# Performance work log

Measured on AMD Instinct MI355X. Metric: run time of the kernel, lower is better.

Reference implementation:

```python
import jax, jax.numpy as jnp
import numpy as np

N_NODES = 150000
N_EDGES = 2400000


def gcn_conv(x, W, b, src, dst, n):
    """PyG GCNConv: add self-loops, symmetric D^-1/2 A_hat D^-1/2 norm, x@W then scatter-sum, + bias."""
    h = x @ W  # [N, out]
    loop = jnp.arange(n)
    s = jnp.concatenate([src, loop])
    d = jnp.concatenate([dst, loop])
    deg = jax.ops.segment_sum(jnp.ones(s.shape, dtype=h.dtype), d, num_segments=n)
    dis = jnp.where(deg > 0, jax.lax.rsqrt(jnp.maximum(deg, 1e-12)), 0.0)
    norm = dis[s] * dis[d]  # [E+N]
    out = jax.ops.segment_sum(h[s] * norm[:, None], d, num_segments=n)
    return out + b


def setup_inputs() -> dict:
    key = jax.random.key(0)
    ks = jax.random.split(key, 16)
    d = 32
    inp = {
        "x": jax.random.normal(ks[0], (N_NODES, 2), dtype=jnp.float32),
        "edge_index": jax.random.randint(ks[1], (2, N_EDGES), 0, N_NODES, dtype=jnp.int64),
        "fc1_w": jax.random.normal(ks[2], (2, d), dtype=jnp.float32) * 0.5,
        "fc1_b": jax.random.normal(ks[3], (d,), dtype=jnp.float32) * 0.1,
        "conv1_w": jax.random.normal(ks[4], (d, d), dtype=jnp.float32) * (1.0 / np.sqrt(d)),
        "conv1_b": jax.random.normal(ks[5], (d,), dtype=jnp.float32) * 0.1,
        "conv2_w": jax.random.normal(ks[6], (d, d), dtype=jnp.float32) * (1.0 / np.sqrt(d)),
        "conv2_b": jax.random.normal(ks[7], (d,), dtype=jnp.float32) * 0.1,
        "conv31_w": jax.random.normal(ks[8], (d, d), dtype=jnp.float32) * (1.0 / np.sqrt(d)),
        "conv31_b": jax.random.normal(ks[9], (d,), dtype=jnp.float32) * 0.1,
        "conv32_w": jax.random.normal(ks[10], (d, d), dtype=jnp.float32) * (1.0 / np.sqrt(d)),
        "conv32_b": jax.random.normal(ks[11], (d,), dtype=jnp.float32) * 0.1,
        "fc21_w": jax.random.normal(ks[12], (d, 1), dtype=jnp.float32) * (1.0 / np.sqrt(d)),
        "fc21_b": jax.random.normal(ks[13], (1,), dtype=jnp.float32) * 0.1,
        "fc22_w": jax.random.normal(ks[14], (d, 1), dtype=jnp.float32) * (1.0 / np.sqrt(d)),
        "fc22_b": jax.random.normal(ks[15], (1,), dtype=jnp.float32) * 0.1,
    }
    return inp


def reference(x, edge_index, fc1_w, fc1_b, conv1_w, conv1_b, conv2_w, conv2_b,
              conv31_w, conv31_b, conv32_w, conv32_b, fc21_w, fc21_b, fc22_w, fc22_b):
    n = x.shape[0]
    src, dst = edge_index[0], edge_index[1]
    h = jax.nn.relu(x @ fc1_w + fc1_b)
    h = jax.nn.relu(gcn_conv(h, conv1_w, conv1_b, src, dst, n))
    h = jax.nn.relu(gcn_conv(h, conv2_w, conv2_b, src, dst, n))
    x1 = jax.nn.relu(gcn_conv(h, conv31_w, conv31_b, src, dst, n)) @ fc21_w + fc21_b
    x2 = jax.nn.relu(gcn_conv(h, conv32_w, conv32_b, src, dst, n)) @ fc22_w + fc22_b
    return jnp.concatenate([x1, x2], axis=1)  # [N, 2]
```

## Files before the change

### kernel.cpp

```cpp
#include <hip/hip_runtime.h>

#define N_NODES 150000
#define N_EDGES 2400000
#define D 32
#define NBUCK 1172
#define CHUNK 4096
#define NCHK 586
#define CSR_CAP (N_EDGES + 3 * N_NODES + 64)

__global__ __launch_bounds__(256) void kA_hist(const int* __restrict__ dst,
                                               int* __restrict__ cnt) {
    __shared__ int bins[NBUCK];
    int t = threadIdx.x;
    for (int k = t; k < NBUCK; k += 256) bins[k] = 0;
    __syncthreads();
    int e0 = blockIdx.x * CHUNK;
#pragma unroll
    for (int r = 0; r < CHUNK / 256; ++r) {
        int e = e0 + r * 256 + t;
        if (e < N_EDGES) atomicAdd(&bins[dst[e] >> 7], 1);
    }
    __syncthreads();
    for (int k = t; k < NBUCK; k += 256) cnt[blockIdx.x * NBUCK + k] = bins[k];
}

__global__ __launch_bounds__(256) void kS1(int* __restrict__ cnt, int* __restrict__ bstart) {
    __shared__ int tile[8][33];
    __shared__ int carry[32];
    int t = threadIdx.x;
    int tl = t & 31, tr = t >> 5;
    int b = blockIdx.x * 32 + tl;
    if (t < 32) carry[t] = 0;
    __syncthreads();
    for (int c0 = 0; c0 < NCHK; c0 += 8) {
        int c = c0 + tr;
        int v = (c < NCHK && b < NBUCK) ? cnt[c * NBUCK + b] : 0;
        tile[tr][tl] = v;
        __syncthreads();
        if (t < 32) {
            int s = carry[t];
#pragma unroll
            for (int r = 0; r < 8; ++r) { int x = tile[r][t]; tile[r][t] = s; s += x; }
            carry[t] = s;
        }
        __syncthreads();
        if (c < NCHK && b < NBUCK) cnt[c * NBUCK + b] = tile[tr][tl];
        __syncthreads();
    }
    if (t < 32 && b < NBUCK) bstart[b] = carry[t];
}

__global__ void k_scan_small(int* __restrict__ a, int m) {
    __shared__ int s[256];
    __shared__ int carry;
    int t = threadIdx.x;
    if (t == 0) carry = 0;
    __syncthreads();
    for (int base = 0; base < m; base += 256) {
        int v = (base + t < m) ? a[base + t] : 0;
        s[t] = v;
        __syncthreads();
        for (int off = 1; off < 256; off <<= 1) {
            int add = (t >= off) ? s[t - off] : 0;
            __syncthreads();
            s[t] += add;
            __syncthreads();
        }
        int c0 = carry;
        if (base + t < m) a[base + t] = c0 + s[t] - v;
        int bsum = s[255];
        __syncthreads();
        if (t == 0) carry = c0 + bsum;
        __syncthreads();
    }
    if (t == 0) a[m] = carry;
}

__global__ __launch_bounds__(256) void kB_scatter(const int* __restrict__ src,
                                                  const int* __restrict__ dst,
                                                  const int* __restrict__ cnt,
                                                  const int* __restrict__ bstart,
                                                  int* __restrict__ ebuf) {
    __shared__ int lofs[NBUCK];
    int t = threadIdx.x;
    for (int k = t; k < NBUCK; k += 256)
        lofs[k] = bstart[k] + cnt[blockIdx.x * NBUCK + k];
    __syncthreads();
    int e0 = blockIdx.x * CHUNK;
#pragma unroll
    for (int r = 0; r < CHUNK / 256; ++r) {
        int e = e0 + r * 256 + t;
        if (e < N_EDGES) {
            int d = dst[e];
            int p = atomicAdd(&lofs[d >> 7], 1);
            ebuf[p] = src[e] | ((d & 127) << 18);
        }
    }
}

__global__ __launch_bounds__(256) void kC1(const int* __restrict__ ebuf,
                                           const int* __restrict__ bstart,
                                           const float2* __restrict__ x,
                                           int* __restrict__ deg,
                                           float* __restrict__ dis,
                                           float4* __restrict__ xd,
                                           int* __restrict__ pbase) {
    __shared__ int hist[128];
    __shared__ int sc[128];
    int b = blockIdx.x, t = threadIdx.x;
    if (t < 128) hist[t] = 0;
    __syncthreads();
    int s0 = bstart[b], s1 = bstart[b + 1];
    for (int e = s0 + t; e < s1; e += 256) atomicAdd(&hist[ebuf[e] >> 18], 1);
    __syncthreads();
    int i = b * 128 + t;
    if (t < 128) {
        int dv = hist[t];
        if (i < N_NODES) {
            deg[i] = dv;
            float dz = rsqrtf((float)dv + 1.0f);
            dis[i] = dz;
            float2 xv = x[i];
            xd[i] = make_float4(xv.x, xv.y, dz, 0.f);
        } else if (i == N_NODES) {
            xd[i] = make_float4(0.f, 0.f, 0.f, 0.f);
        }
        sc[t] = (i < N_NODES) ? ((dv + 3) & ~3) : 0;
    }
    __syncthreads();
    for (int s = 64; s > 0; s >>= 1) {
        if (t < s) sc[t] += sc[t + s];
        __syncthreads();
    }
    if (t == 0) pbase[b] = sc[0];
}

__global__ __launch_bounds__(256) void kC3(const int* __restrict__ ebuf,
                                           const int* __restrict__ bstart,
                                           const int* __restrict__ deg,
                                           const int* __restrict__ pbase,
                                           int* __restrict__ csr,
                                           int* __restrict__ irow,
                                           float* __restrict__ HA,
                                           float* __restrict__ HB) {
    __shared__ int sc[128];
    __shared__ int loff[128];
    __shared__ int pos[128];
    int b = blockIdx.x, t = threadIdx.x;
    if (b == 0) {
        if (t == 0) irow[N_NODES] = pbase[NBUCK];
        if (t < 64) csr[pbase[NBUCK] + t] = N_NODES;
        if (t >= 64 && t < 96) HA[(size_t)N_NODES * D + (t - 64)] = 0.f;
        if (t >= 96 && t < 128) HB[(size_t)N_NODES * D + (t - 96)] = 0.f;
    }
    int i = b * 128 + t;
    int dv = 0, pad = 0;
    if (t < 128) {
        dv = (i < N_NODES) ? deg[i] : 0;
        pad = (dv + 3) & ~3;
        sc[t] = pad;
        pos[t] = 0;
    }
    __syncthreads();
    for (int off = 1; off < 128; off <<= 1) {
        int add = 0;
        if (t < 128 && t >= off) add = sc[t - off];
        __syncthreads();
        if (t < 128) sc[t] += add;
        __syncthreads();
    }
    int base = pbase[b];
    if (t < 128) {
        loff[t] = sc[t] - pad;
        if (i < N_NODES) irow[i] = base + loff[t];
    }
    __syncthreads();
    int s0 = bstart[b], s1 = bstart[b + 1];
    for (int e = s0 + t; e < s1; e += 256) {
        int v = ebuf[e];
        int dl = v >> 18;
        int p = atomicAdd(&pos[dl], 1);
        csr[base + loff[dl] + p] = v & 0x3FFFF;
    }
    __syncthreads();
    if (t < 128 && i < N_NODES) {
        int st = base + loff[t] + dv, en = base + loff[t] + pad;
        for (int q = st; q < en; ++q) csr[q] = N_NODES;
    }
}

__global__ __launch_bounds__(256) void k_layer1f(const float4* __restrict__ xd,
                                                 const int* __restrict__ row,
                                                 const int* __restrict__ csr,
                                                 const float* __restrict__ W,
                                                 const float* __restrict__ bf,
                                                 const float* __restrict__ Wc,
                                                 const float* __restrict__ bc,
                                                 float* __restrict__ hout) {
    __shared__ float4 stage[8][16];
    __shared__ float arow[8][32];
    int g = threadIdx.x >> 5, l = threadIdx.x & 31, f = l;
    int t = blockIdx.x * 256 + threadIdx.x;
    int i = t >> 5;
    if (i >= N_NODES) return;
    float w0 = W[f], w1 = W[D + f], bb = bf[f];
    float wcol[D];
#pragma unroll
    for (int k = 0; k < D; ++k) wcol[k] = Wc[k * D + f];
    float4 sv = xd[i];
    float hs = fmaf(sv.x, w0, fmaf(sv.y, w1, bb));
    hs = hs > 0.f ? hs : 0.f;
    float a = hs * sv.z;
    int rs = row[i], re = row[i + 1];
    int j0 = rs;
    int cs = csr[j0 + (l & 15)];
    while (j0 < re) {
        int nxt = csr[j0 + 16 + (l & 15)];
        if (l < 16) {
            int s2 = (j0 + l < re) ? cs : N_NODES;
            stage[g][l] = xd[s2];
        }
#pragma unroll
        for (int it = 0; it < 4; ++it) {
            if (j0 + it * 4 >= re) break;
            float4 v0 = stage[g][it * 4 + 0];
            float4 v1 = stage[g][it * 4 + 1];
            float4 v2 = stage[g][it * 4 + 2];
            float4 v3 = stage[g][it * 4 + 3];
            float h0 = fmaf(v0.x, w0, fmaf(v0.y, w1, bb)); h0 = h0 > 0.f ? h0 : 0.f;
            float h1 = fmaf(v1.x, w0, fmaf(v1.y, w1, bb)); h1 = h1 > 0.f ? h1 : 0.f;
            float h2 = fmaf(v2.x, w0, fmaf(v2.y, w1, bb)); h2 = h2 > 0.f ? h2 : 0.f;
            float h3 = fmaf(v3.x, w0, fmaf(v3.y, w1, bb)); h3 = h3 > 0.f ? h3 : 0.f;
            a = fmaf(h0, v0.z, a);
            a = fmaf(h1, v1.z, a);
            a = fmaf(h2, v2.z, a);
            a = fmaf(h3, v3.z, a);
        }
        cs = nxt;
        j0 += 16;
    }
    float di = sv.z;
    a *= di;
    arow[g][f] = a;
    float acc = 0.f;
#pragma unroll
    for (int q = 0; q < 8; ++q) {
        float4 aq = ((const float4*)arow[g])[q];
        acc = fmaf(aq.x, wcol[4 * q + 0],
              fmaf(aq.y, wcol[4 * q + 1],
              fmaf(aq.z, wcol[4 * q + 2],
              fmaf(aq.w, wcol[4 * q + 3], acc))));
    }
    float v = acc + bc[f];
    v = v > 0.f ? v : 0.f;
    hout[t] = v * di;
}

__global__ __launch_bounds__(256) void k_layer(const float* __restrict__ hsc,
                                               const int* __restrict__ row,
                                               const int* __restrict__ csr,
                                               const float* __restrict__ dis,
                                               const float* __restrict__ W,
                                               const float* __restrict__ b,
                                               float* __restrict__ hout) {
    __shared__ float arow[16][32];
    int g = threadIdx.x >> 5, l = threadIdx.x & 31, f = l;
    int gg = blockIdx.x * 8 + g;
    int iA = gg * 2, iB = iA + 1;
    float wcol[D];
#pragma unroll
    for (int k = 0; k < D; ++k) wcol[k] = W[k * D + f];
    int c = l & 7, l16 = l & 15, sub = l >> 3;
    const float4* rowf4 = (const float4*)hsc;
    int rsA = row[iA], mid = row[iB], reB = row[iB + 1];
    float4 aA = make_float4(0.f, 0.f, 0.f, 0.f);
    float4 aB = make_float4(0.f, 0.f, 0.f, 0.f);
    int jA = rsA, jB = mid;
    int csA = csr[jA + l16], csB = csr[jB + l16];
    while (jA < mid && jB < reB) {
        int nA = csr[jA + 16 + l16], nB = csr[jB + 16 + l16];
        float4 vA[4], vB[4];
#pragma unroll
        for (int it = 0; it < 4; ++it)
            if (jA + it * 4 < mid) { int s = __shfl(csA, it * 4 + sub, 32); vA[it] = rowf4[s * 8 + c]; }
#pragma unroll
        for (int it = 0; it < 4; ++it)
            if (jB + it * 4 < reB) { int s = __shfl(csB, it * 4 + sub, 32); vB[it] = rowf4[s * 8 + c]; }
#pragma unroll
        for (int it = 0; it < 4; ++it) {
            if (jA + it * 4 < mid) { aA.x += vA[it].x; aA.y += vA[it].y; aA.z += vA[it].z; aA.w += vA[it].w; }
            if (jB + it * 4 < reB) { aB.x += vB[it].x; aB.y += vB[it].y; aB.z += vB[it].z; aB.w += vB[it].w; }
        }
        csA = nA; csB = nB; jA += 16; jB += 16;
    }
    while (jA < mid) {
        int nA = csr[jA + 16 + l16];
        float4 vA[4];
#pragma unroll
        for (int it = 0; it < 4; ++it)
            if (jA + it * 4 < mid) { int s = __shfl(csA, it * 4 + sub, 32); vA[it] = rowf4[s * 8 + c]; }
#pragma unroll
        for (int it = 0; it < 4; ++it)
            if (jA + it * 4 < mid) { aA.x += vA[it].x; aA.y += vA[it].y; aA.z += vA[it].z; aA.w += vA[it].w; }
        csA = nA; jA += 16;
    }
    while (jB < reB) {
        int nB = csr[jB + 16 + l16];
        float4 vB[4];
#pragma unroll
        for (int it = 0; it < 4; ++it)
            if (jB + it * 4 < reB) { int s = __shfl(csB, it * 4 + sub, 32); vB[it] = rowf4[s * 8 + c]; }
#pragma unroll
        for (int it = 0; it < 4; ++it)
            if (jB + it * 4 < reB) { aB.x += vB[it].x; aB.y += vB[it].y; aB.z += vB[it].z; aB.w += vB[it].w; }
        csB = nB; jB += 16;
    }
    aA.x += __shfl_xor(aA.x, 8, 32);  aA.y += __shfl_xor(aA.y, 8, 32);
    aA.z += __shfl_xor(aA.z, 8, 32);  aA.w += __shfl_xor(aA.w, 8, 32);
    aA.x += __shfl_xor(aA.x, 16, 32); aA.y += __shfl_xor(aA.y, 16, 32);
    aA.z += __shfl_xor(aA.z, 16, 32); aA.w += __shfl_xor(aA.w, 16, 32);
    aB.x += __shfl_xor(aB.x, 8, 32);  aB.y += __shfl_xor(aB.y, 8, 32);
    aB.z += __shfl_xor(aB.z, 8, 32);  aB.w += __shfl_xor(aB.w, 8, 32);
    aB.x += __shfl_xor(aB.x, 16, 32); aB.y += __shfl_xor(aB.y, 16, 32);
    aB.z += __shfl_xor(aB.z, 16, 32); aB.w += __shfl_xor(aB.w, 16, 32);
    float4 svA = rowf4[iA * 8 + c], svB = rowf4[iB * 8 + c];
    float diA = dis[iA], diB = dis[iB];
    aA.x = (aA.x + svA.x) * diA; aA.y = (aA.y + svA.y) * diA;
    aA.z = (aA.z + svA.z) * diA; aA.w = (aA.w + svA.w) * diA;
    aB.x = (aB.x + svB.x) * diB; aB.y = (aB.y + svB.y) * diB;
    aB.z = (aB.z + svB.z) * diB; aB.w = (aB.w + svB.w) * diB;
    if (l < 8) ((float4*)arow[g * 2])[l] = aA;
    else if (l < 16) ((float4*)arow[g * 2 + 1])[l - 8] = aB;
    float accA = 0.f, accB = 0.f;
#pragma unroll
    for (int q = 0; q < 8; ++q) {
        float4 qa = ((const float4*)arow[g * 2])[q];
        float4 qb = ((const float4*)arow[g * 2 + 1])[q];
        accA = fmaf(qa.x, wcol[4 * q + 0],
               fmaf(qa.y, wcol[4 * q + 1],
               fmaf(qa.z, wcol[4 * q + 2],
               fmaf(qa.w, wcol[4 * q + 3], accA))));
        accB = fmaf(qb.x, wcol[4 * q + 0],
               fmaf(qb.y, wcol[4 * q + 1],
               fmaf(qb.z, wcol[4 * q + 2],
               fmaf(qb.w, wcol[4 * q + 3], accB))));
    }
    float vA_ = accA + b[f]; vA_ = vA_ > 0.f ? vA_ : 0.f;
    float vB_ = accB + b[f]; vB_ = vB_ > 0.f ? vB_ : 0.f;
    hout[iA * D + f] = vA_ * diA;
    hout[iB * D + f] = vB_ * diB;
}

__global__ __launch_bounds__(256) void k_heads(
    const float* __restrict__ hsc, const int* __restrict__ row,
    const int* __restrict__ csr, const float* __restrict__ dis,
    const float* __restrict__ W1, const float* __restrict__ b1,
    const float* __restrict__ W2, const float* __restrict__ b2,
    const float* __restrict__ fw1, const float* __restrict__ fb1,
    const float* __restrict__ fw2, const float* __restrict__ fb2,
    float* __restrict__ out) {
    __shared__ float arow[16][32];
    int g = threadIdx.x >> 5, l = threadIdx.x & 31, f = l;
    int gg = blockIdx.x * 8 + g;
    int iA = gg * 2, iB = iA + 1;
    float wc1[D], wc2[D];
#pragma unroll
    for (int k = 0; k < D; ++k) { wc1[k] = W1[k * D + f]; wc2[k] = W2[k * D + f]; }
    int c = l & 7, l16 = l & 15, sub = l >> 3;
    const float4* rowf4 = (const float4*)hsc;
    int rsA = row[iA], mid = row[iB], reB = row[iB + 1];
    float4 aA = make_float4(0.f, 0.f, 0.f, 0.f);
    float4 aB = make_float4(0.f, 0.f, 0.f, 0.f);
    int jA = rsA, jB = mid;
    int csA = csr[jA + l16], csB = csr[jB + l16];
    while (jA < mid && jB < reB) {
        int nA = csr[jA + 16 + l16], nB = csr[jB + 16 + l16];
        float4 vA[4], vB[4];
#pragma unroll
        for (int it = 0; it < 4; ++it)
            if (jA + it * 4 < mid) { int s = __shfl(csA, it * 4 + sub, 32); vA[it] = rowf4[s * 8 + c]; }
#pragma unroll
        for (int it = 0; it < 4; ++it)
            if (jB + it * 4 < reB) { int s = __shfl(csB, it * 4 + sub, 32); vB[it] = rowf4[s * 8 + c]; }
#pragma unroll
        for (int it = 0; it < 4; ++it) {
            if (jA + it * 4 < mid) { aA.x += vA[it].x; aA.y += vA[it].y; aA.z += vA[it].z; aA.w += vA[it].w; }
            if (jB + it * 4 < reB) { aB.x += vB[it].x; aB.y += vB[it].y; aB.z += vB[it].z; aB.w += vB[it].w; }
        }
        csA = nA; csB = nB; jA += 16; jB += 16;
    }
    while (jA < mid) {
        int nA = csr[jA + 16 + l16];
        float4 vA[4];
#pragma unroll
        for (int it = 0; it < 4; ++it)
            if (jA + it * 4 < mid) { int s = __shfl(csA, it * 4 + sub, 32); vA[it] = rowf4[s * 8 + c]; }
#pragma unroll
        for (int it = 0; it < 4; ++it)
            if (jA + it * 4 < mid) { aA.x += vA[it].x; aA.y += vA[it].y; aA.z += vA[it].z; aA.w += vA[it].w; }
        csA = nA; jA += 16;
    }
    while (jB < reB) {
        int nB = csr[jB + 16 + l16];
        float4 vB[4];
#pragma unroll
        for (int it = 0; it < 4; ++it)
            if (jB + it * 4 < reB) { int s = __shfl(csB, it * 4 + sub, 32); vB[it] = rowf4[s * 8 + c]; }
#pragma unroll
        for (int it = 0; it < 4; ++it)
            if (jB + it * 4 < reB) { aB.x += vB[it].x; aB.y += vB[it].y; aB.z += vB[it].z; aB.w += vB[it].w; }
        csB = nB; jB += 16;
    }
    aA.x += __shfl_xor(aA.x, 8, 32);  aA.y += __shfl_xor(aA.y, 8, 32);
    aA.z += __shfl_xor(aA.z, 8, 32);  aA.w += __shfl_xor(aA.w, 8, 32);
    aA.x += __shfl_xor(aA.x, 16, 32); aA.y += __shfl_xor(aA.y, 16, 32);
    aA.z += __shfl_xor(aA.z, 16, 32); aA.w += __shfl_xor(aA.w, 16, 32);
    aB.x += __shfl_xor(aB.x, 8, 32);  aB.y += __shfl_xor(aB.y, 8, 32);
    aB.z += __shfl_xor(aB.z, 8, 32);  aB.w += __shfl_xor(aB.w, 8, 32);
    aB.x += __shfl_xor(aB.x, 16, 32); aB.y += __shfl_xor(aB.y, 16, 32);
    aB.z += __shfl_xor(aB.z, 16, 32); aB.w += __shfl_xor(aB.w, 16, 32);
    float4 svA = rowf4[iA * 8 + c], svB = rowf4[iB * 8 + c];
    float diA = dis[iA], diB = dis[iB];
    aA.x = (aA.x + svA.x) * diA; aA.y = (aA.y + svA.y) * diA;
    aA.z = (aA.z + svA.z) * diA; aA.w = (aA.w + svA.w) * diA;
    aB.x = (aB.x + svB.x) * diB; aB.y = (aB.y + svB.y) * diB;
    aB.z = (aB.z + svB.z) * diB; aB.w = (aB.w + svB.w) * diB;
    if (l < 8) ((float4*)arow[g * 2])[l] = aA;
    else if (l < 16) ((float4*)arow[g * 2 + 1])[l - 8] = aB;
    float a1A = 0.f, a2A = 0.f, a1B = 0.f, a2B = 0.f;
#pragma unroll
    for (int q = 0; q < 8; ++q) {
        float4 qa = ((const float4*)arow[g * 2])[q];
        float4 qb = ((const float4*)arow[g * 2 + 1])[q];
        a1A = fmaf(qa.x, wc1[4 * q + 0], fmaf(qa.y, wc1[4 * q + 1],
              fmaf(qa.z, wc1[4 * q + 2], fmaf(qa.w, wc1[4 * q + 3], a1A))));
        a2A = fmaf(qa.x, wc2[4 * q + 0], fmaf(qa.y, wc2[4 * q + 1],
              fmaf(qa.z, wc2[4 * q + 2], fmaf(qa.w, wc2[4 * q + 3], a2A))));
        a1B = fmaf(qb.x, wc1[4 * q + 0], fmaf(qb.y, wc1[4 * q + 1],
              fmaf(qb.z, wc1[4 * q + 2], fmaf(qb.w, wc1[4 * q + 3], a1B))));
        a2B = fmaf(qb.x, wc2[4 * q + 0], fmaf(qb.y, wc2[4 * q + 1],
              fmaf(qb.z, wc2[4 * q + 2], fmaf(qb.w, wc2[4 * q + 3], a2B))));
    }
    float v1A = a1A + b1[f]; v1A = (v1A > 0.f ? v1A : 0.f) * fw1[f];
    float v2A = a2A + b2[f]; v2A = (v2A > 0.f ? v2A : 0.f) * fw2[f];
    float v1B = a1B + b1[f]; v1B = (v1B > 0.f ? v1B : 0.f) * fw1[f];
    float v2B = a2B + b2[f]; v2B = (v2B > 0.f ? v2B : 0.f) * fw2[f];
#pragma unroll
    for (int o = 16; o > 0; o >>= 1) {
        v1A += __shfl_down(v1A, o, 32);
        v2A += __shfl_down(v2A, o, 32);
        v1B += __shfl_down(v1B, o, 32);
        v2B += __shfl_down(v2B, o, 32);
    }
    if (l == 0) {
        float4 o4 = make_float4(v1A + fb1[0], v2A + fb2[0], v1B + fb1[0], v2B + fb2[0]);
        *(float4*)&out[iA * 2] = o4;
    }
}

extern "C" void kernel_launch(void* const* d_in, const int* in_sizes, int n_in,
                              void* d_out, int out_size, void* d_ws, size_t ws_size,
                              hipStream_t stream) {
    const float* x       = (const float*)d_in[0];
    const int*   eidx    = (const int*)d_in[1];
    const float* fc1_w   = (const float*)d_in[2];
    const float* fc1_b   = (const float*)d_in[3];
    const float* conv1_w = (const float*)d_in[4];
    const float* conv1_b = (const float*)d_in[5];
    const float* conv2_w = (const float*)d_in[6];
    const float* conv2_b = (const float*)d_in[7];
    const float* c31_w   = (const float*)d_in[8];
    const float* c31_b   = (const float*)d_in[9];
    const float* c32_w   = (const float*)d_in[10];
    const float* c32_b   = (const float*)d_in[11];
    const float* fc21_w  = (const float*)d_in[12];
    const float* fc21_b  = (const float*)d_in[13];
    const float* fc22_w  = (const float*)d_in[14];
    const float* fc22_b  = (const float*)d_in[15];
    float* out = (float*)d_out;

    const int* src = eidx;
    const int* dst = eidx + N_EDGES;

    int*   wsb    = (int*)d_ws;
    int*   csr    = wsb;
    int*   irow   = wsb + 2850064;
    int*   bstart = wsb + 3000068;
    int*   pbase  = wsb + 3001242;
    float* dis    = (float*)(wsb + 3002416);
    float* HA     = (float*)(wsb + 3152416);
    float* HB     = (float*)(wsb + 7952448);
    int*    cnt  = (int*)HA;
    int*    ebuf = (int*)HA + 700000;
    float4* xd   = (float4*)((int*)HA + 3100016);
    int*    deg  = (int*)HB;

    const int BLK = 256;
    const int gL  = (N_NODES * D + BLK - 1) / BLK;
    const int gL2 = N_NODES / 16;

    kA_hist<<<NCHK, BLK, 0, stream>>>(dst, cnt);
    kS1<<<(NBUCK + 31) / 32, BLK, 0, stream>>>(cnt, bstart);
    k_scan_small<<<1, BLK, 0, stream>>>(bstart, NBUCK);
    kB_scatter<<<NCHK, BLK, 0, stream>>>(src, dst, cnt, bstart, ebuf);
    kC1<<<NBUCK, BLK, 0, stream>>>(ebuf, bstart, (const float2*)x, deg, dis, xd, pbase);
    k_scan_small<<<1, BLK, 0, stream>>>(pbase, NBUCK);
    kC3<<<NBUCK, BLK, 0, stream>>>(ebuf, bstart, deg, pbase, csr, irow, HA, HB);

    k_layer1f<<<gL, BLK, 0, stream>>>(xd, irow, csr, fc1_w, fc1_b, conv1_w, conv1_b, HB);
    k_layer<<<gL2, BLK, 0, stream>>>(HB, irow, csr, dis, conv2_w, conv2_b, HA);
    k_heads<<<gL2, BLK, 0, stream>>>(HA, irow, csr, dis, c31_w, c31_b, c32_w, c32_b,
                                     fc21_w, fc21_b, fc22_w, fc22_b, out);
}
```

Measured before the change: 257.6 us.

## Process four nodes per warp and load weights on the fly instead of register arrays

All three layer kernels now have each 32-lane group handle four nodes in two passes, and the launch uses a quarter as many blocks. The per-thread weight-column register arrays are dropped; weights are read from memory inside the dense transform loop, which lowers register pressure and could raise occupancy. Layer 1 now gathers two nodes' neighbours at once, using both 16-lane halves to stage features into shared memory. The cost is more weight loads (expected to be cached) and less parallelism per launch.

```diff
diff --git a/kernel.cpp b/kernel.cpp
--- a/kernel.cpp
+++ b/kernel.cpp
@@ -197,63 +197,88 @@
                                                  const float* __restrict__ Wc,
                                                  const float* __restrict__ bc,
                                                  float* __restrict__ hout) {
-    __shared__ float4 stage[8][16];
-    __shared__ float arow[8][32];
+    __shared__ float4 stage[8][2][16];
+    __shared__ float arow[16][32];
     int g = threadIdx.x >> 5, l = threadIdx.x & 31, f = l;
-    int t = blockIdx.x * 256 + threadIdx.x;
-    int i = t >> 5;
-    if (i >= N_NODES) return;
+    int gg = blockIdx.x * 8 + g;
+    if (gg * 4 >= N_NODES) return;
     float w0 = W[f], w1 = W[D + f], bb = bf[f];
-    float wcol[D];
-#pragma unroll
-    for (int k = 0; k < D; ++k) wcol[k] = Wc[k * D + f];
-    float4 sv = xd[i];
-    float hs = fmaf(sv.x, w0, fmaf(sv.y, w1, bb));
-    hs = hs > 0.f ? hs : 0.f;
-    float a = hs * sv.z;
-    int rs = row[i], re = row[i + 1];
-    int j0 = rs;
-    int cs = csr[j0 + (l & 15)];
-    while (j0 < re) {
-        int nxt = csr[j0 + 16 + (l & 15)];
-        if (l < 16) {
-            int s2 = (j0 + l < re) ? cs : N_NODES;
-            stage[g][l] = xd[s2];
-        }
-#pragma unroll
-        for (int it = 0; it < 4; ++it) {
-            if (j0 + it * 4 >= re) break;
-            float4 v0 = stage[g][it * 4 + 0];
-            float4 v1 = stage[g][it * 4 + 1];
-            float4 v2 = stage[g][it * 4 + 2];
-            float4 v3 = stage[g][it * 4 + 3];
-            float h0 = fmaf(v0.x, w0, fmaf(v0.y, w1, bb)); h0 = h0 > 0.f ? h0 : 0.f;
-            float h1 = fmaf(v1.x, w0, fmaf(v1.y, w1, bb)); h1 = h1 > 0.f ? h1 : 0.f;
-            float h2 = fmaf(v2.x, w0, fmaf(v2.y, w1, bb)); h2 = h2 > 0.f ? h2 : 0.f;
-            float h3 = fmaf(v3.x, w0, fmaf(v3.y, w1, bb)); h3 = h3 > 0.f ? h3 : 0.f;
-            a = fmaf(h0, v0.z, a);
-            a = fmaf(h1, v1.z, a);
-            a = fmaf(h2, v2.z, a);
-            a = fmaf(h3, v3.z, a);
-        }
-        cs = nxt;
-        j0 += 16;
-    }
-    float di = sv.z;
-    a *= di;
-    arow[g][f] = a;
-    float acc = 0.f;
-#pragma unroll
-    for (int q = 0; q < 8; ++q) {
-        float4 aq = ((const float4*)arow[g])[q];
-        acc = fmaf(aq.x, wcol[4 * q + 0],
-              fmaf(aq.y, wcol[4 * q + 1],
-              fmaf(aq.z, wcol[4 * q + 2],
-              fmaf(aq.w, wcol[4 * q + 3], acc))));
-    }
-    float v = acc + bc[f];
-    v = v > 0.f ? v : 0.f;
-    hout[t] = v * di;
+    int half = l >> 4, li = l & 15;
+#pragma unroll
+    for (int rep = 0; rep < 2; ++rep) {
+        int iA = gg * 4 + rep * 2, iB = iA + 1;
+        float4 svA = xd[iA], svB = xd[iB];
+        float hsA = fmaf(svA.x, w0, fmaf(svA.y, w1, bb)); hsA = hsA > 0.f ? hsA : 0.f;
+        float hsB = fmaf(svB.x, w0, fmaf(svB.y, w1, bb)); hsB = hsB > 0.f ? hsB : 0.f;
+        float aA = hsA * svA.z, aB = hsB * svB.z;
+        int rsA = row[iA], mid = row[iB], reB = row[iB + 1];
+        int jA = rsA, jB = mid;
+        int mye = half ? reB : mid;
+        int slot0 = (half ? jB : jA) + li;
+        int cs = csr[slot0];
+        cs = (slot0 < mye) ? cs : N_NODES;
+        while (jA < mid || jB < reB) {
+            stage[g][half][li] = xd[cs];
+            int nslot = (half ? jB : jA) + 16 + li;
+            int ncs = csr[nslot];
+            ncs = (nslot < mye) ? ncs : N_NODES;
+            if (jA < mid) {
+#pragma unroll
+                for (int it = 0; it < 4; ++it) {
+                    if (jA + it * 4 < mid) {
+                        float4 v0 = stage[g][0][it * 4 + 0];
+                        float4 v1 = stage[g][0][it * 4 + 1];
+                        float4 v2 = stage[g][0][it * 4 + 2];
+                        float4 v3 = stage[g][0][it * 4 + 3];
+                        float h0 = fmaf(v0.x, w0, fmaf(v0.y, w1, bb)); h0 = h0 > 0.f ? h0 : 0.f;
+                        float h1 = fmaf(v1.x, w0, fmaf(v1.y, w1, bb)); h1 = h1 > 0.f ? h1 : 0.f;
+                        float h2 = fmaf(v2.x, w0, fmaf(v2.y, w1, bb)); h2 = h2 > 0.f ? h2 : 0.f;
+                        float h3 = fmaf(v3.x, w0, fmaf(v3.y, w1, bb)); h3 = h3 > 0.f ? h3 : 0.f;
+                        aA = fmaf(h0, v0.z, aA); aA = fmaf(h1, v1.z, aA);
+                        aA = fmaf(h2, v2.z, aA); aA = fmaf(h3, v3.z, aA);
+                    }
+                }
+                jA += 16;
+            }
+            if (jB < reB) {
+#pragma unroll
+                for (int it = 0; it < 4; ++it) {
+                    if (jB + it * 4 < reB) {
+                        float4 v0 = stage[g][1][it * 4 + 0];
+                        float4 v1 = stage[g][1][it * 4 + 1];
+                        float4 v2 = stage[g][1][it * 4 + 2];
+                        float4 v3 = stage[g][1][it * 4 + 3];
+                        float h0 = fmaf(v0.x, w0, fmaf(v0.y, w1, bb)); h0 = h0 > 0.f ? h0 : 0.f;
+                        float h1 = fmaf(v1.x, w0, fmaf(v1.y, w1, bb)); h1 = h1 > 0.f ? h1 : 0.f;
+                        float h2 = fmaf(v2.x, w0, fmaf(v2.y, w1, bb)); h2 = h2 > 0.f ? h2 : 0.f;
+                        float h3 = fmaf(v3.x, w0, fmaf(v3.y, w1, bb)); h3 = h3 > 0.f ? h3 : 0.f;
+                        aB = fmaf(h0, v0.z, aB); aB = fmaf(h1, v1.z, aB);
+                        aB = fmaf(h2, v2.z, aB); aB = fmaf(h3, v3.z, aB);
+                    }
+                }
+                jB += 16;
+            }
+            cs = ncs;
+        }
+        aA *= svA.z; aB *= svB.z;
+        arow[g * 2][f] = aA;
+        arow[g * 2 + 1][f] = aB;
+        float accA = 0.f, accB = 0.f;
+#pragma unroll
+        for (int q = 0; q < 8; ++q) {
+            float4 qa = ((const float4*)arow[g * 2])[q];
+            float4 qb = ((const float4*)arow[g * 2 + 1])[q];
+            float wq0 = Wc[(4 * q + 0) * D + f], wq1 = Wc[(4 * q + 1) * D + f];
+            float wq2 = Wc[(4 * q + 2) * D + f], wq3 = Wc[(4 * q + 3) * D + f];
+            accA = fmaf(qa.x, wq0, fmaf(qa.y, wq1, fmaf(qa.z, wq2, fmaf(qa.w, wq3, accA))));
+            accB = fmaf(qb.x, wq0, fmaf(qb.y, wq1, fmaf(qb.z, wq2, fmaf(qb.w, wq3, accB))));
+        }
+        float bcf = bc[f];
+        float vA = accA + bcf; vA = vA > 0.f ? vA : 0.f;
+        float vB = accB + bcf; vB = vB > 0.f ? vB : 0.f;
+        hout[iA * D + f] = vA * svA.z;
+        hout[iB * D + f] = vB * svB.z;
+    }
 }
 
 __global__ __launch_bounds__(256) void k_layer(const float* __restrict__ hsc,
@@ -266,89 +291,87 @@
     __shared__ float arow[16][32];
     int g = threadIdx.x >> 5, l = threadIdx.x & 31, f = l;
     int gg = blockIdx.x * 8 + g;
-    int iA = gg * 2, iB = iA + 1;
-    float wcol[D];
-#pragma unroll
-    for (int k = 0; k < D; ++k) wcol[k] = W[k * D + f];
+    if (gg * 4 >= N_NODES) return;
     int c = l & 7, l16 = l & 15, sub = l >> 3;
     const float4* rowf4 = (const float4*)hsc;
-    int rsA = row[iA], mid = row[iB], reB = row[iB + 1];
-    float4 aA = make_float4(0.f, 0.f, 0.f, 0.f);
-    float4 aB = make_float4(0.f, 0.f, 0.f, 0.f);
-    int jA = rsA, jB = mid;
-    int csA = csr[jA + l16], csB = csr[jB + l16];
-    while (jA < mid && jB < reB) {
-        int nA = csr[jA + 16 + l16], nB = csr[jB + 16 + l16];
-        float4 vA[4], vB[4];
-#pragma unroll
-        for (int it = 0; it < 4; ++it)
-            if (jA + it * 4 < mid) { int s = __shfl(csA, it * 4 + sub, 32); vA[it] = rowf4[s * 8 + c]; }
-#pragma unroll
-        for (int it = 0; it < 4; ++it)
-            if (jB + it * 4 < reB) { int s = __shfl(csB, it * 4 + sub, 32); vB[it] = rowf4[s * 8 + c]; }
-#pragma unroll
-        for (int it = 0; it < 4; ++it) {
-            if (jA + it * 4 < mid) { aA.x += vA[it].x; aA.y += vA[it].y; aA.z += vA[it].z; aA.w += vA[it].w; }
-            if (jB + it * 4 < reB) { aB.x += vB[it].x; aB.y += vB[it].y; aB.z += vB[it].z; aB.w += vB[it].w; }
-        }
-        csA = nA; csB = nB; jA += 16; jB += 16;
-    }
-    while (jA < mid) {
-        int nA = csr[jA + 16 + l16];
-        float4 vA[4];
-#pragma unroll
-        for (int it = 0; it < 4; ++it)
-            if (jA + it * 4 < mid) { int s = __shfl(csA, it * 4 + sub, 32); vA[it] = rowf4[s * 8 + c]; }
-#pragma unroll
-        for (int it = 0; it < 4; ++it)
-            if (jA + it * 4 < mid) { aA.x += vA[it].x; aA.y += vA[it].y; aA.z += vA[it].z; aA.w += vA[it].w; }
-        csA = nA; jA += 16;
-    }
-    while (jB < reB) {
-        int nB = csr[jB + 16 + l16];
-        float4 vB[4];
-#pragma unroll
-        for (int it = 0; it < 4; ++it)
-            if (jB + it * 4 < reB) { int s = __shfl(csB, it * 4 + sub, 32); vB[it] = rowf4[s * 8 + c]; }
-#pragma unroll
-        for (int it = 0; it < 4; ++it)
-            if (jB + it * 4 < reB) { aB.x += vB[it].x; aB.y += vB[it].y; aB.z += vB[it].z; aB.w += vB[it].w; }
-        csB = nB; jB += 16;
-    }
-    aA.x += __shfl_xor(aA.x, 8, 32);  aA.y += __shfl_xor(aA.y, 8, 32);
-    aA.z += __shfl_xor(aA.z, 8, 32);  aA.w += __shfl_xor(aA.w, 8, 32);
-    aA.x += __shfl_xor(aA.x, 16, 32); aA.y += __shfl_xor(aA.y, 16, 32);
-    aA.z += __shfl_xor(aA.z, 16, 32); aA.w += __shfl_xor(aA.w, 16, 32);
-    aB.x += __shfl_xor(aB.x, 8, 32);  aB.y += __shfl_xor(aB.y, 8, 32);
-    aB.z += __shfl_xor(aB.z, 8, 32);  aB.w += __shfl_xor(aB.w, 8, 32);
-    aB.x += __shfl_xor(aB.x, 16, 32); aB.y += __shfl_xor(aB.y, 16, 32);
-    aB.z += __shfl_xor(aB.z, 16, 32); aB.w += __shfl_xor(aB.w, 16, 32);
-    float4 svA = rowf4[iA * 8 + c], svB = rowf4[iB * 8 + c];
-    float diA = dis[iA], diB = dis[iB];
-    aA.x = (aA.x + svA.x) * diA; aA.y = (aA.y + svA.y) * diA;
-    aA.z = (aA.z + svA.z) * diA; aA.w = (aA.w + svA.w) * diA;
-    aB.x = (aB.x + svB.x) * diB; aB.y = (aB.y + svB.y) * diB;
-    aB.z = (aB.z + svB.z) * diB; aB.w = (aB.w + svB.w) * diB;
-    if (l < 8) ((float4*)arow[g * 2])[l] = aA;
-    else if (l < 16) ((float4*)arow[g * 2 + 1])[l - 8] = aB;
-    float accA = 0.f, accB = 0.f;
-#pragma unroll
-    for (int q = 0; q < 8; ++q) {
-        float4 qa = ((const float4*)arow[g * 2])[q];
-        float4 qb = ((const float4*)arow[g * 2 + 1])[q];
-        accA = fmaf(qa.x, wcol[4 * q + 0],
-               fmaf(qa.y, wcol[4 * q + 1],
-               fmaf(qa.z, wcol[4 * q + 2],
-               fmaf(qa.w, wcol[4 * q + 3], accA))));
-        accB = fmaf(qb.x, wcol[4 * q + 0],
-               fmaf(qb.y, wcol[4 * q + 1],
-               fmaf(qb.z, wcol[4 * q + 2],
-               fmaf(qb.w, wcol[4 * q + 3], accB))));
-    }
-    float vA_ = accA + b[f]; vA_ = vA_ > 0.f ? vA_ : 0.f;
-    float vB_ = accB + b[f]; vB_ = vB_ > 0.f ? vB_ : 0.f;
-    hout[iA * D + f] = vA_ * diA;
-    hout[iB * D + f] = vB_ * diB;
+#pragma unroll
+    for (int rep = 0; rep < 2; ++rep) {
+        int iA = gg * 4 + rep * 2, iB = iA + 1;
+        int rsA = row[iA], mid = row[iB], reB = row[iB + 1];
+        float4 aA = make_float4(0.f, 0.f, 0.f, 0.f);
+        float4 aB = make_float4(0.f, 0.f, 0.f, 0.f);
+        int jA = rsA, jB = mid;
+        int csA = csr[jA + l16], csB = csr[jB + l16];
+        while (jA < mid && jB < reB) {
+            int nA = csr[jA + 16 + l16], nB = csr[jB + 16 + l16];
+            float4 vA[4], vB[4];
+#pragma unroll
+            for (int it = 0; it < 4; ++it)
+                if (jA + it * 4 < mid) { int s = __shfl(csA, it * 4 + sub, 32); vA[it] = rowf4[s * 8 + c]; }
+#pragma unroll
+            for (int it = 0; it < 4; ++it)
+                if (jB + it * 4 < reB) { int s = __shfl(csB, it * 4 + sub, 32); vB[it] = rowf4[s * 8 + c]; }
+#pragma unroll
+            for (int it = 0; it < 4; ++it) {
+                if (jA + it * 4 < mid) { aA.x += vA[it].x; aA.y += vA[it].y; aA.z += vA[it].z; aA.w += vA[it].w; }
+                if (jB + it * 4 < reB) { aB.x += vB[it].x; aB.y += vB[it].y; aB.z += vB[it].z; aB.w += vB[it].w; }
+            }
+            csA = nA; csB = nB; jA += 16; jB += 16;
+        }
+        while (jA < mid) {
+            int nA = csr[jA + 16 + l16];
+            float4 vA[4];
+#pragma unroll
+            for (int it = 0; it < 4; ++it)
+                if (jA + it * 4 < mid) { int s = __shfl(csA, it * 4 + sub, 32); vA[it] = rowf4[s * 8 + c]; }
+#pragma unroll
+            for (int it = 0; it < 4; ++it)
+                if (jA + it * 4 < mid) { aA.x += vA[it].x; aA.y += vA[it].y; aA.z += vA[it].z; aA.w += vA[it].w; }
+            csA = nA; jA += 16;
+        }
+        while (jB < reB) {
+            int nB = csr[jB + 16 + l16];
+            float4 vB[4];
+#pragma unroll
+            for (int it = 0; it < 4; ++it)
+                if (jB + it * 4 < reB) { int s = __shfl(csB, it * 4 + sub, 32); vB[it] = rowf4[s * 8 + c]; }
+#pragma unroll
+            for (int it = 0; it < 4; ++it)
+                if (jB + it * 4 < reB) { aB.x += vB[it].x; aB.y += vB[it].y; aB.z += vB[it].z; aB.w += vB[it].w; }
+            csB = nB; jB += 16;
+        }
+        aA.x += __shfl_xor(aA.x, 8, 32);  aA.y += __shfl_xor(aA.y, 8, 32);
+        aA.z += __shfl_xor(aA.z, 8, 32);  aA.w += __shfl_xor(aA.w, 8, 32);
+        aA.x += __shfl_xor(aA.x, 16, 32); aA.y += __shfl_xor(aA.y, 16, 32);
+        aA.z += __shfl_xor(aA.z, 16, 32); aA.w += __shfl_xor(aA.w, 16, 32);
+        aB.x += __shfl_xor(aB.x, 8, 32);  aB.y += __shfl_xor(aB.y, 8, 32);
+        aB.z += __shfl_xor(aB.z, 8, 32);  aB.w += __shfl_xor(aB.w, 8, 32);
+        aB.x += __shfl_xor(aB.x, 16, 32); aB.y += __shfl_xor(aB.y, 16, 32);
+        aB.z += __shfl_xor(aB.z, 16, 32); aB.w += __shfl_xor(aB.w, 16, 32);
+        float4 svA = rowf4[iA * 8 + c], svB = rowf4[iB * 8 + c];
+        float diA = dis[iA], diB = dis[iB];
+        aA.x = (aA.x + svA.x) * diA; aA.y = (aA.y + svA.y) * diA;
+        aA.z = (aA.z + svA.z) * diA; aA.w = (aA.w + svA.w) * diA;
+        aB.x = (aB.x + svB.x) * diB; aB.y = (aB.y + svB.y) * diB;
+        aB.z = (aB.z + svB.z) * diB; aB.w = (aB.w + svB.w) * diB;
+        if (l < 8) ((float4*)arow[g * 2])[l] = aA;
+        else if (l < 16) ((float4*)arow[g * 2 + 1])[l - 8] = aB;
+        float accA = 0.f, accB = 0.f;
+#pragma unroll
+        for (int q = 0; q < 8; ++q) {
+            float4 qa = ((const float4*)arow[g * 2])[q];
+            float4 qb = ((const float4*)arow[g * 2 + 1])[q];
+            float wq0 = W[(4 * q + 0) * D + f], wq1 = W[(4 * q + 1) * D + f];
+            float wq2 = W[(4 * q + 2) * D + f], wq3 = W[(4 * q + 3) * D + f];
+            accA = fmaf(qa.x, wq0, fmaf(qa.y, wq1, fmaf(qa.z, wq2, fmaf(qa.w, wq3, accA))));
+            accB = fmaf(qb.x, wq0, fmaf(qb.y, wq1, fmaf(qb.z, wq2, fmaf(qb.w, wq3, accB))));
+        }
+        float bb = b[f];
+        float vA_ = accA + bb; vA_ = vA_ > 0.f ? vA_ : 0.f;
+        float vB_ = accB + bb; vB_ = vB_ > 0.f ? vB_ : 0.f;
+        hout[iA * D + f] = vA_ * diA;
+        hout[iB * D + f] = vB_ * diB;
+    }
 }
 
 __global__ __launch_bounds__(256) void k_heads(
@@ -362,99 +385,100 @@
     __shared__ float arow[16][32];
     int g = threadIdx.x >> 5, l = threadIdx.x & 31, f = l;
     int gg = blockIdx.x * 8 + g;
-    int iA = gg * 2, iB = iA + 1;
-    float wc1[D], wc2[D];
-#pragma unroll
-    for (int k = 0; k < D; ++k) { wc1[k] = W1[k * D + f]; wc2[k] = W2[k * D + f]; }
+    if (gg * 4 >= N_NODES) return;
     int c = l & 7, l16 = l & 15, sub = l >> 3;
     const float4* rowf4 = (const float4*)hsc;
-    int rsA = row[iA], mid = row[iB], reB = row[iB + 1];
-    float4 aA = make_float4(0.f, 0.f, 0.f, 0.f);
-    float4 aB = make_float4(0.f, 0.f, 0.f, 0.f);
-    int jA = rsA, jB = mid;
-    int csA = csr[jA + l16], csB = csr[jB + l16];
-    while (jA < mid && jB < reB) {
-        int nA = csr[jA + 16 + l16], nB = csr[jB + 16 + l16];
-        float4 vA[4], vB[4];
-#pragma unroll
-        for (int it = 0; it < 4; ++it)
-            if (jA + it * 4 < mid) { int s = __shfl(csA, it * 4 + sub, 32); vA[it] = rowf4[s * 8 + c]; }
-#pragma unroll
-        for (int it = 0; it < 4; ++it)
-            if (jB + it * 4 < reB) { int s = __shfl(csB, it * 4 + sub, 32); vB[it] = rowf4[s * 8 + c]; }
-#pragma unroll
-        for (int it = 0; it < 4; ++it) {
-            if (jA + it * 4 < mid) { aA.x += vA[it].x; aA.y += vA[it].y; aA.z += vA[it].z; aA.w += vA[it].w; }
-            if (jB + it * 4 < reB) { aB.x += vB[it].x; aB.y += vB[it].y; aB.z += vB[it].z; aB.w += vB[it].w; }
-        }
-        csA = nA; csB = nB; jA += 16; jB += 16;
-    }
-    while (jA < mid) {
-        int nA = csr[jA + 16 + l16];
-        float4 vA[4];
-#pragma unroll
-        for (int it = 0; it < 4; ++it)
-            if (jA + it * 4 < mid) { int s = __shfl(csA, it * 4 + sub, 32); vA[it] = rowf4[s * 8 + c]; }
-#pragma unroll
-        for (int it = 0; it < 4; ++it)
-            if (jA + it * 4 < mid) { aA.x += vA[it].x; aA.y += vA[it].y; aA.z += vA[it].z; aA.w += vA[it].w; }
-        csA = nA; jA += 16;
-    }
-    while (jB < reB) {
-        int nB = csr[jB + 16 + l16];
-        float4 vB[4];
-#pragma unroll
-        for (int it = 0; it < 4; ++it)
-            if (jB + it * 4 < reB) { int s = __shfl(csB, it * 4 + sub, 32); vB[it] = rowf4[s * 8 + c]; }
-#pragma unroll
-        for (int it = 0; it < 4; ++it)
-            if (jB + it * 4 < reB) { aB.x += vB[it].x; aB.y += vB[it].y; aB.z += vB[it].z; aB.w += vB[it].w; }
-        csB = nB; jB += 16;
-    }
-    aA.x += __shfl_xor(aA.x, 8, 32);  aA.y += __shfl_xor(aA.y, 8, 32);
-    aA.z += __shfl_xor(aA.z, 8, 32);  aA.w += __shfl_xor(aA.w, 8, 32);
-    aA.x += __shfl_xor(aA.x, 16, 32); aA.y += __shfl_xor(aA.y, 16, 32);
-    aA.z += __shfl_xor(aA.z, 16, 32); aA.w += __shfl_xor(aA.w, 16, 32);
-    aB.x += __shfl_xor(aB.x, 8, 32);  aB.y += __shfl_xor(aB.y, 8, 32);
-    aB.z += __shfl_xor(aB.z, 8, 32);  aB.w += __shfl_xor(aB.w, 8, 32);
-    aB.x += __shfl_xor(aB.x, 16, 32); aB.y += __shfl_xor(aB.y, 16, 32);
-    aB.z += __shfl_xor(aB.z, 16, 32); aB.w += __shfl_xor(aB.w, 16, 32);
-    float4 svA = rowf4[iA * 8 + c], svB = rowf4[iB * 8 + c];
-    float diA = dis[iA], diB = dis[iB];
-    aA.x = (aA.x + svA.x) * diA; aA.y = (aA.y + svA.y) * diA;
-    aA.z = (aA.z + svA.z) * diA; aA.w = (aA.w + svA.w) * diA;
-    aB.x = (aB.x + svB.x) * diB; aB.y = (aB.y + svB.y) * diB;
-    aB.z = (aB.z + svB.z) * diB; aB.w = (aB.w + svB.w) * diB;
-    if (l < 8) ((float4*)arow[g * 2])[l] = aA;
-    else if (l < 16) ((float4*)arow[g * 2 + 1])[l - 8] = aB;
-    float a1A = 0.f, a2A = 0.f, a1B = 0.f, a2B = 0.f;
-#pragma unroll
-    for (int q = 0; q < 8; ++q) {
-        float4 qa = ((const float4*)arow[g * 2])[q];
-        float4 qb = ((const float4*)arow[g * 2 + 1])[q];
-        a1A = fmaf(qa.x, wc1[4 * q + 0], fmaf(qa.y, wc1[4 * q + 1],
-              fmaf(qa.z, wc1[4 * q + 2], fmaf(qa.w, wc1[4 * q + 3], a1A))));
-        a2A = fmaf(qa.x, wc2[4 * q + 0], fmaf(qa.y, wc2[4 * q + 1],
-              fmaf(qa.z, wc2[4 * q + 2], fmaf(qa.w, wc2[4 * q + 3], a2A))));
-        a1B = fmaf(qb.x, wc1[4 * q + 0], fmaf(qb.y, wc1[4 * q + 1],
-              fmaf(qb.z, wc1[4 * q + 2], fmaf(qb.w, wc1[4 * q + 3], a1B))));
-        a2B = fmaf(qb.x, wc2[4 * q + 0], fmaf(qb.y, wc2[4 * q + 1],
-              fmaf(qb.z, wc2[4 * q + 2], fmaf(qb.w, wc2[4 * q + 3], a2B))));
-    }
-    float v1A = a1A + b1[f]; v1A = (v1A > 0.f ? v1A : 0.f) * fw1[f];
-    float v2A = a2A + b2[f]; v2A = (v2A > 0.f ? v2A : 0.f) * fw2[f];
-    float v1B = a1B + b1[f]; v1B = (v1B > 0.f ? v1B : 0.f) * fw1[f];
-    float v2B = a2B + b2[f]; v2B = (v2B > 0.f ? v2B : 0.f) * fw2[f];
-#pragma unroll
-    for (int o = 16; o > 0; o >>= 1) {
-        v1A += __shfl_down(v1A, o, 32);
-        v2A += __shfl_down(v2A, o, 32);
-        v1B += __shfl_down(v1B, o, 32);
-        v2B += __shfl_down(v2B, o, 32);
-    }
-    if (l == 0) {
-        float4 o4 = make_float4(v1A + fb1[0], v2A + fb2[0], v1B + fb1[0], v2B + fb2[0]);
-        *(float4*)&out[iA * 2] = o4;
+#pragma unroll
+    for (int rep = 0; rep < 2; ++rep) {
+        int iA = gg * 4 + rep * 2, iB = iA + 1;
+        int rsA = row[iA], mid = row[iB], reB = row[iB + 1];
+        float4 aA = make_float4(0.f, 0.f, 0.f, 0.f);
+        float4 aB = make_float4(0.f, 0.f, 0.f, 0.f);
+        int jA = rsA, jB = mid;
+        int csA = csr[jA + l16], csB = csr[jB + l16];
+        while (jA < mid && jB < reB) {
+            int nA = csr[jA + 16 + l16], nB = csr[jB + 16 + l16];
+            float4 vA[4], vB[4];
+#pragma unroll
+            for (int it = 0; it < 4; ++it)
+                if (jA + it * 4 < mid) { int s = __shfl(csA, it * 4 + sub, 32); vA[it] = rowf4[s * 8 + c]; }
+#pragma unroll
+            for (int it = 0; it < 4; ++it)
+                if (jB + it * 4 < reB) { int s = __shfl(csB, it * 4 + sub, 32); vB[it] = rowf4[s * 8 + c]; }
+#pragma unroll
+            for (int it = 0; it < 4; ++it) {
+                if (jA + it * 4 < mid) { aA.x += vA[it].x; aA.y += vA[it].y; aA.z += vA[it].z; aA.w += vA[it].w; }
+                if (jB + it * 4 < reB) { aB.x += vB[it].x; aB.y += vB[it].y; aB.z += vB[it].z; aB.w += vB[it].w; }
+            }
+            csA = nA; csB = nB; jA += 16; jB += 16;
+        }
+        while (jA < mid) {
+            int nA = csr[jA + 16 + l16];
+            float4 vA[4];
+#pragma unroll
+            for (int it = 0; it < 4; ++it)
+                if (jA + it * 4 < mid) { int s = __shfl(csA, it * 4 + sub, 32); vA[it] = rowf4[s * 8 + c]; }
+#pragma unroll
+            for (int it = 0; it < 4; ++it)
+                if (jA + it * 4 < mid) { aA.x += vA[it].x; aA.y += vA[it].y; aA.z += vA[it].z; aA.w += vA[it].w; }
+            csA = nA; jA += 16;
+        }
+        while (jB < reB) {
+            int nB = csr[jB + 16 + l16];
+            float4 vB[4];
+#pragma unroll
+            for (int it = 0; it < 4; ++it)
+                if (jB + it * 4 < reB) { int s = __shfl(csB, it * 4 + sub, 32); vB[it] = rowf4[s * 8 + c]; }
+#pragma unroll
+            for (int it = 0; it < 4; ++it)
+                if (jB + it * 4 < reB) { aB.x += vB[it].x; aB.y += vB[it].y; aB.z += vB[it].z; aB.w += vB[it].w; }
+            csB = nB; jB += 16;
+        }
+        aA.x += __shfl_xor(aA.x, 8, 32);  aA.y += __shfl_xor(aA.y, 8, 32);
+        aA.z += __shfl_xor(aA.z, 8, 32);  aA.w += __shfl_xor(aA.w, 8, 32);
+        aA.x += __shfl_xor(aA.x, 16, 32); aA.y += __shfl_xor(aA.y, 16, 32);
+        aA.z += __shfl_xor(aA.z, 16, 32); aA.w += __shfl_xor(aA.w, 16, 32);
+        aB.x += __shfl_xor(aB.x, 8, 32);  aB.y += __shfl_xor(aB.y, 8, 32);
+        aB.z += __shfl_xor(aB.z, 8, 32);  aB.w += __shfl_xor(aB.w, 8, 32);
+        aB.x += __shfl_xor(aB.x, 16, 32); aB.y += __shfl_xor(aB.y, 16, 32);
+        aB.z += __shfl_xor(aB.z, 16, 32); aB.w += __shfl_xor(aB.w, 16, 32);
+        float4 svA = rowf4[iA * 8 + c], svB = rowf4[iB * 8 + c];
+        float diA = dis[iA], diB = dis[iB];
+        aA.x = (aA.x + svA.x) * diA; aA.y = (aA.y + svA.y) * diA;
+        aA.z = (aA.z + svA.z) * diA; aA.w = (aA.w + svA.w) * diA;
+        aB.x = (aB.x + svB.x) * diB; aB.y = (aB.y + svB.y) * diB;
+        aB.z = (aB.z + svB.z) * diB; aB.w = (aB.w + svB.w) * diB;
+        if (l < 8) ((float4*)arow[g * 2])[l] = aA;
+        else if (l < 16) ((float4*)arow[g * 2 + 1])[l - 8] = aB;
+        float a1A = 0.f, a2A = 0.f, a1B = 0.f, a2B = 0.f;
+#pragma unroll
+        for (int q = 0; q < 8; ++q) {
+            float4 qa = ((const float4*)arow[g * 2])[q];
+            float4 qb = ((const float4*)arow[g * 2 + 1])[q];
+            float u0 = W1[(4 * q + 0) * D + f], u1 = W1[(4 * q + 1) * D + f];
+            float u2 = W1[(4 * q + 2) * D + f], u3 = W1[(4 * q + 3) * D + f];
+            float t0 = W2[(4 * q + 0) * D + f], t1 = W2[(4 * q + 1) * D + f];
+            float t2 = W2[(4 * q + 2) * D + f], t3 = W2[(4 * q + 3) * D + f];
+            a1A = fmaf(qa.x, u0, fmaf(qa.y, u1, fmaf(qa.z, u2, fmaf(qa.w, u3, a1A))));
+            a2A = fmaf(qa.x, t0, fmaf(qa.y, t1, fmaf(qa.z, t2, fmaf(qa.w, t3, a2A))));
+            a1B = fmaf(qb.x, u0, fmaf(qb.y, u1, fmaf(qb.z, u2, fmaf(qb.w, u3, a1B))));
+            a2B = fmaf(qb.x, t0, fmaf(qb.y, t1, fmaf(qb.z, t2, fmaf(qb.w, t3, a2B))));
+        }
+        float v1A = a1A + b1[f]; v1A = (v1A > 0.f ? v1A : 0.f) * fw1[f];
+        float v2A = a2A + b2[f]; v2A = (v2A > 0.f ? v2A : 0.f) * fw2[f];
+        float v1B = a1B + b1[f]; v1B = (v1B > 0.f ? v1B : 0.f) * fw1[f];
+        float v2B = a2B + b2[f]; v2B = (v2B > 0.f ? v2B : 0.f) * fw2[f];
+#pragma unroll
+        for (int o = 16; o > 0; o >>= 1) {
+            v1A += __shfl_down(v1A, o, 32);
+            v2A += __shfl_down(v2A, o, 32);
+            v1B += __shfl_down(v1B, o, 32);
+            v2B += __shfl_down(v2B, o, 32);
+        }
+        if (l == 0) {
+            float4 o4 = make_float4(v1A + fb1[0], v2A + fb2[0], v1B + fb1[0], v2B + fb2[0]);
+            *(float4*)&out[iA * 2] = o4;
+        }
     }
 }
 
@@ -496,8 +520,7 @@
     int*    deg  = (int*)HB;
 
     const int BLK = 256;
-    const int gL  = (N_NODES * D + BLK - 1) / BLK;
-    const int gL2 = N_NODES / 16;
+    const int gL  = (N_NODES + 31) / 32;
 
     kA_hist<<<NCHK, BLK, 0, stream>>>(dst, cnt);
     kS1<<<(NBUCK + 31) / 32, BLK, 0, stream>>>(cnt, bstart);
@@ -508,7 +531,7 @@
     kC3<<<NBUCK, BLK, 0, stream>>>(ebuf, bstart, deg, pbase, csr, irow, HA, HB);
 
     k_layer1f<<<gL, BLK, 0, stream>>>(xd, irow, csr, fc1_w, fc1_b, conv1_w, conv1_b, HB);
-    k_layer<<<gL2, BLK, 0, stream>>>(HB, irow, csr, dis, conv2_w, conv2_b, HA);
-    k_heads<<<gL2, BLK, 0, stream>>>(HA, irow, csr, dis, c31_w, c31_b, c32_w, c32_b,
-                                     fc21_w, fc21_b, fc22_w, fc22_b, out);
-}
+    k_layer<<<gL, BLK, 0, stream>>>(HB, irow, csr, dis, conv2_w, conv2_b, HA);
+    k_heads<<<gL, BLK, 0, stream>>>(HA, irow, csr, dis, c31_w, c31_b, c32_w, c32_b,
+                                    fc21_w, fc21_b, fc22_w, fc22_b, out);
+}
```

Result: slower. 271.7 us (+5.5%).
